# Kernel optimization log

Hardware: AMD Instinct MI355X
Metric: run time of the kernel (lower is better)

The kernel has to match this reference:

```python
import jax, jax.numpy as jnp
import numpy as np

EMBED_DIM = 768
N_HEADS = 12
MLP_HID = 3072  # mlp_ratio 4.0
LN_EPS = 1e-6


def setup_inputs() -> dict:
    key = jax.random.key(0)
    ks = jax.random.split(key, 12)
    B, N, C = 4, 2048, EMBED_DIM
    s = 0.02
    return {
        "x": jax.random.normal(ks[0], (B, N, C), jnp.float32),
        "mask": jnp.ones((B, N), jnp.int32),
        "ln1_g": jnp.ones((C,), jnp.float32),
        "ln1_b": jnp.zeros((C,), jnp.float32),
        "qkv_w": jax.random.normal(ks[1], (C, 3 * C), jnp.float32) * s,
        "qkv_b": jnp.zeros((3 * C,), jnp.float32),
        "proj_w": jax.random.normal(ks[2], (C, C), jnp.float32) * s,
        "proj_b": jnp.zeros((C,), jnp.float32),
        "ln2_g": jnp.ones((C,), jnp.float32),
        "ln2_b": jnp.zeros((C,), jnp.float32),
        "fc1_w": jax.random.normal(ks[3], (C, MLP_HID), jnp.float32) * s,
        "fc1_b": jnp.zeros((MLP_HID,), jnp.float32),
        "fc2_w": jax.random.normal(ks[4], (MLP_HID, C), jnp.float32) * s,
        "fc2_b": jnp.zeros((C,), jnp.float32),
    }


def _layernorm(x, g, b):
    mu = jnp.mean(x, axis=-1, keepdims=True)
    var = jnp.mean(jnp.square(x - mu), axis=-1, keepdims=True)
    return (x - mu) * jax.lax.rsqrt(var + LN_EPS) * g + b


def _block(x, mask, ln1_g, ln1_b, qkv_w, qkv_b, proj_w, proj_b,
           ln2_g, ln2_b, fc1_w, fc1_b, fc2_w, fc2_b):
    B, N, C = x.shape
    H, D = N_HEADS, C // N_HEADS
    scale = D ** -0.5

    # --- attention (pre-norm) ---
    h = _layernorm(x, ln1_g, ln1_b)
    qkv = h @ qkv_w + qkv_b                      # [B,N,3C]
    qkv = qkv.reshape(B, N, 3, H, D).transpose(2, 0, 3, 1, 4)
    q, k, v = qkv[0], qkv[1], qkv[2]             # [B,H,N,D]
    scores = jnp.einsum("bhqd,bhkd->bhqk", q, k * scale)
    # 2-D mask path: (bsz, seq) -> (bsz, 1, seq, 1), mask queries
    m = mask[:, None, :, None]
    scores = jnp.where(m == 0, jnp.finfo(scores.dtype).min, scores)
    attn = jax.nn.softmax(scores, axis=-1)
    vals = jnp.einsum("bhqk,bhkd->bhqd", attn, v)
    vals = vals.transpose(0, 2, 1, 3).reshape(B, N, C)
    x = x + (vals @ proj_w + proj_b)

    # --- MLP (pre-norm, GELU exact) ---
    h = _layernorm(x, ln2_g, ln2_b)
    h = jax.nn.gelu(h @ fc1_w + fc1_b, approximate=False)
    x = x + (h @ fc2_w + fc2_b)
    return x


def reference(x, mask, ln1_g, ln1_b, qkv_w, qkv_b, proj_w, proj_b,
              ln2_g, ln2_b, fc1_w, fc1_b, fc2_w, fc2_b):
    return _block(x, mask, ln1_g, ln1_b, qkv_w, qkv_b, proj_w, proj_b,
                  ln2_g, ln2_b, fc1_w, fc1_b, fc2_w, fc2_b)
```

## Files before the change

### kernel.cpp

```cpp
#include <hip/hip_runtime.h>
#include <hip/hip_bf16.h>
#include <math.h>

using bf16 = __hip_bfloat16;
typedef short s16x8 __attribute__((ext_vector_type(8)));
typedef float f32x4 __attribute__((ext_vector_type(4)));
typedef float f32x16 __attribute__((ext_vector_type(16)));

#define LOG2E 1.4426950408889634f
#define QSCALE 0.18033688f

__device__ inline unsigned short f2bf(float f) {
    bf16 h = __float2bfloat16(f);
    return __builtin_bit_cast(unsigned short, h);
}

__device__ inline void gload_lds16(const void* g, void* l) {
    __builtin_amdgcn_global_load_lds(
        (const __attribute__((address_space(1))) void*)g,
        (__attribute__((address_space(3))) void*)l, 16, 0, 0);
}

__device__ inline unsigned cvtpk(float lo, float hi) {
    unsigned r;
    asm("v_cvt_pk_bf16_f32 %0, %1, %2" : "=v"(r) : "v"(lo), "v"(hi));
    return r;
}

__device__ inline s16x8 build_pfrag(float p0, float p1, float p2, float p3,
                                    float p4, float p5, float p6, float p7) {
    unsigned w01 = cvtpk(p0, p1);
    unsigned w23 = cvtpk(p2, p3);
    unsigned w45 = cvtpk(p4, p5);
    unsigned w67 = cvtpk(p6, p7);
    asm volatile("v_permlane32_swap_b32 %0, %1" : "+v"(w01), "+v"(w45));
    asm volatile("v_permlane32_swap_b32 %0, %1" : "+v"(w23), "+v"(w67));
    int4 t = {(int)w01, (int)w23, (int)w45, (int)w67};
    return __builtin_bit_cast(s16x8, t);
}

__global__ __launch_bounds__(256) void transpose_all(
    const float* __restrict__ qkv_w, const float* __restrict__ proj_w,
    const float* __restrict__ fc1_w, const float* __restrict__ fc2_w,
    bf16* __restrict__ Wqkv, bf16* __restrict__ Wproj,
    bf16* __restrict__ Wfc1, bf16* __restrict__ Wfc2)
{
    int t = blockIdx.x;
    const float* in;
    bf16* out;
    int K, N, xt;
    if (t < 1728)      { in = qkv_w;  out = Wqkv;  K = 768;  N = 2304; xt = 72; }
    else if (t < 2304) { in = proj_w; out = Wproj; K = 768;  N = 768;  xt = 24; t -= 1728; }
    else if (t < 4608) { in = fc1_w;  out = Wfc1;  K = 768;  N = 3072; xt = 96; t -= 2304; }
    else               { in = fc2_w;  out = Wfc2;  K = 3072; N = 768;  xt = 24; t -= 4608; }
    const int bx = (t % xt) * 32;
    const int by = (t / xt) * 32;

    __shared__ float tile[32][33];
    const int tx = threadIdx.x, ty = threadIdx.y;
    #pragma unroll
    for (int i = 0; i < 32; i += 8)
        tile[ty + i][tx] = in[(size_t)(by + ty + i) * N + bx + tx];
    __syncthreads();
    #pragma unroll
    for (int i = 0; i < 32; i += 8)
        out[(size_t)(bx + ty + i) * K + by + tx] = __float2bfloat16(tile[tx][ty + i]);
}

__global__ __launch_bounds__(256) void ln_kernel(
    const float* __restrict__ x, const float* __restrict__ g,
    const float* __restrict__ bb, bf16* __restrict__ out)
{
    const int row = blockIdx.x;
    const float* xr = x + (size_t)row * 768;
    float v[3];
    float s = 0.f, s2 = 0.f;
    #pragma unroll
    for (int i = 0; i < 3; ++i) {
        v[i] = xr[threadIdx.x + i * 256];
        s += v[i];
        s2 += v[i] * v[i];
    }
    #pragma unroll
    for (int off = 1; off < 64; off <<= 1) {
        s += __shfl_xor(s, off);
        s2 += __shfl_xor(s2, off);
    }
    __shared__ float rs[4], rs2[4];
    const int wave = threadIdx.x >> 6;
    if ((threadIdx.x & 63) == 0) { rs[wave] = s; rs2[wave] = s2; }
    __syncthreads();
    s = rs[0] + rs[1] + rs[2] + rs[3];
    s2 = rs2[0] + rs2[1] + rs2[2] + rs2[3];
    const float mu = s * (1.f / 768.f);
    const float var = s2 * (1.f / 768.f) - mu * mu;
    const float r = rsqrtf(var + 1e-6f);
    bf16* orow = out + (size_t)row * 768;
    #pragma unroll
    for (int i = 0; i < 3; ++i) {
        const int col = threadIdx.x + i * 256;
        orow[col] = __float2bfloat16((v[i] - mu) * r * g[col] + bb[col]);
    }
}

template <int EPI>
__global__ __launch_bounds__(256) void gemm_bt(
    const bf16* __restrict__ A, const bf16* __restrict__ Bt,
    const float* __restrict__ bias,
    void* __restrict__ outp, const int* __restrict__ mask,
    bf16* __restrict__ Qb, bf16* __restrict__ Kb, bf16* __restrict__ Vt,
    int M, int N, int K)
{
    __shared__ alignas(16) char smem[32768];
    char* As = smem;
    char* Bs = smem + 16384;
    const int tid = threadIdx.x;
    const int lane = tid & 63;
    const int wave = tid >> 6;
    const int wm = wave >> 1, wn = wave & 1;
    const int lr = lane & 15, lg = lane >> 4;
    const int bm = blockIdx.x, bn = blockIdx.y;

    f32x4 acc[4][4] = {};

    const size_t a_row0 = (size_t)bm * 128;
    const size_t b_row0 = (size_t)bn * 128;

    for (int kt = 0; kt < K; kt += 64) {
        #pragma unroll
        for (int i = 0; i < 4; ++i) {
            const int id = tid + i * 256;
            const int row = id >> 3, c = id & 7;
            const int cs = (c ^ (row & 7)) * 8;
            gload_lds16(A + (a_row0 + row) * K + kt + cs, As + id * 16);
            gload_lds16(Bt + (b_row0 + row) * K + kt + cs, Bs + id * 16);
        }
        __syncthreads();
        #pragma unroll
        for (int ks = 0; ks < 2; ++ks) {
            s16x8 af[4], bfr[4];
            #pragma unroll
            for (int mf = 0; mf < 4; ++mf) {
                const int row = wm * 64 + mf * 16 + lr;
                const int c = ks * 4 + lg;
                af[mf] = *reinterpret_cast<const s16x8*>(As + row * 128 + ((c ^ (row & 7)) * 16));
            }
            #pragma unroll
            for (int nf = 0; nf < 4; ++nf) {
                const int row = wn * 64 + nf * 16 + lr;
                const int c = ks * 4 + lg;
                bfr[nf] = *reinterpret_cast<const s16x8*>(Bs + row * 128 + ((c ^ (row & 7)) * 16));
            }
            #pragma unroll
            for (int mf = 0; mf < 4; ++mf)
                #pragma unroll
                for (int nf = 0; nf < 4; ++nf)
                    acc[mf][nf] = __builtin_amdgcn_mfma_f32_16x16x32_bf16(
                        af[mf], bfr[nf], acc[mf][nf], 0, 0, 0);
        }
        __syncthreads();
    }

    if (EPI == 3) {
        const int rq = bn / 6;
        const int bb_ = bm >> 4;
        if (rq == 2) {
            char* Ws = smem + wave * 8192;
            #pragma unroll
            for (int nf = 0; nf < 4; ++nf) {
                const int cl = nf * 16 + lr;
                const int gn = bn * 128 + wn * 64 + nf * 16 + lr;
                const float bs = bias[gn];
                #pragma unroll
                for (int mf = 0; mf < 4; ++mf) {
                    unsigned short pk[4];
                    #pragma unroll
                    for (int i = 0; i < 4; ++i) pk[i] = f2bf(acc[mf][nf][i] + bs);
                    const int slot = (2 * mf + (lg >> 1)) ^ (cl & 7);
                    *reinterpret_cast<long long*>(Ws + cl * 128 + slot * 16 + (lg & 1) * 8) =
                        *reinterpret_cast<const long long*>(pk);
                }
            }
            __syncthreads();
            const int nb = (bm * 128 + wm * 64) & 2047;
            const int cb = (bn - 12) * 128 + wn * 64;
            #pragma unroll
            for (int r = 0; r < 8; ++r) {
                const int cl = r * 8 + (lane >> 3);
                const int j = lane & 7;
                const int4 vv = *reinterpret_cast<const int4*>(
                    Ws + cl * 128 + ((j ^ (cl & 7)) * 16));
                const int c = cb + cl;
                const int hh = c >> 6, dd = c & 63;
                *reinterpret_cast<int4*>(
                    Vt + ((size_t)(bb_ * 12 + hh) * 64 + dd) * 2048 + nb + j * 8) = vv;
            }
        } else {
            const int cb = bn * 128 - rq * 768 + wn * 64;
            bf16* dst = (rq == 0) ? Qb : Kb;
            #pragma unroll
            for (int mf = 0; mf < 4; ++mf) {
                #pragma unroll
                for (int i = 0; i < 4; ++i) {
                    const int gm = bm * 128 + wm * 64 + mf * 16 + 4 * lg + i;
                    const int n = gm & 2047;
                    const float msc = (rq == 0) ? (mask[gm] ? QSCALE : 0.f) : 1.f;
                    #pragma unroll
                    for (int nf = 0; nf < 4; ++nf) {
                        const int c = cb + nf * 16 + lr;
                        const int h = c >> 6, d = c & 63;
                        const int gn = bn * 128 + wn * 64 + nf * 16 + lr;
                        const float v = (acc[mf][nf][i] + bias[gn]) * msc;
                        dst[((size_t)(bb_ * 12 + h) * 2048 + n) * 64 + d] =
                            __float2bfloat16(v);
                    }
                }
            }
        }
        return;
    }

    #pragma unroll
    for (int mf = 0; mf < 4; ++mf) {
        #pragma unroll
        for (int i = 0; i < 4; ++i) {
            const int gm = bm * 128 + wm * 64 + mf * 16 + 4 * lg + i;
            #pragma unroll
            for (int nf = 0; nf < 4; ++nf) {
                const int gn = bn * 128 + wn * 64 + nf * 16 + lr;
                float v = acc[mf][nf][i] + bias[gn];
                if (EPI == 2) {
                    const float x3 = v * v * v;
                    const float z = fmaf(x3, 0.044715f, v) * 2.3022080f;
                    const float e = __builtin_amdgcn_exp2f(z);
                    v = v - v * __builtin_amdgcn_rcpf(1.f + e);
                }
                reinterpret_cast<bf16*>(outp)[(size_t)gm * N + gn] = __float2bfloat16(v);
            }
        }
    }
}

__global__ __launch_bounds__(256) void gemm64(
    const bf16* __restrict__ A, const bf16* __restrict__ Bt,
    const float* __restrict__ bias, const float* __restrict__ resid,
    float* __restrict__ outp, int M, int N, int K)
{
    __shared__ alignas(16) char smem[24576];
    char* As = smem;
    char* Bs = smem + 8192;
    const int tid = threadIdx.x;
    const int lane = tid & 63;
    const int wn = tid >> 6;
    const int lr = lane & 15, lg = lane >> 4;
    const int bm = blockIdx.x, bn = blockIdx.y;

    f32x4 acc[4][2] = {};

    const size_t a_row0 = (size_t)bm * 64;
    const size_t b_row0 = (size_t)bn * 128;

    for (int kt = 0; kt < K; kt += 64) {
        #pragma unroll
        for (int i = 0; i < 2; ++i) {
            const int id = tid + i * 256;
            const int row = id >> 3, c = id & 7;
            const int cs = (c ^ (row & 7)) * 8;
            gload_lds16(A + (a_row0 + row) * K + kt + cs, As + id * 16);
        }
        #pragma unroll
        for (int i = 0; i < 4; ++i) {
            const int id = tid + i * 256;
            const int row = id >> 3, c = id & 7;
            const int cs = (c ^ (row & 7)) * 8;
            gload_lds16(Bt + (b_row0 + row) * K + kt + cs, Bs + id * 16);
        }
        __syncthreads();
        #pragma unroll
        for (int ks = 0; ks < 2; ++ks) {
            s16x8 af[4], bfr[2];
            #pragma unroll
            for (int mf = 0; mf < 4; ++mf) {
                const int row = mf * 16 + lr;
                const int c = ks * 4 + lg;
                af[mf] = *reinterpret_cast<const s16x8*>(As + row * 128 + ((c ^ (row & 7)) * 16));
            }
            #pragma unroll
            for (int nf = 0; nf < 2; ++nf) {
                const int row = wn * 32 + nf * 16 + lr;
                const int c = ks * 4 + lg;
                bfr[nf] = *reinterpret_cast<const s16x8*>(Bs + row * 128 + ((c ^ (row & 7)) * 16));
            }
            #pragma unroll
            for (int mf = 0; mf < 4; ++mf)
                #pragma unroll
                for (int nf = 0; nf < 2; ++nf)
                    acc[mf][nf] = __builtin_amdgcn_mfma_f32_16x16x32_bf16(
                        af[mf], bfr[nf], acc[mf][nf], 0, 0, 0);
        }
        __syncthreads();
    }

    #pragma unroll
    for (int mf = 0; mf < 4; ++mf) {
        #pragma unroll
        for (int i = 0; i < 4; ++i) {
            const int gm = bm * 64 + mf * 16 + 4 * lg + i;
            #pragma unroll
            for (int nf = 0; nf < 2; ++nf) {
                const int gn = bn * 128 + wn * 32 + nf * 16 + lr;
                outp[(size_t)gm * N + gn] =
                    acc[mf][nf][i] + bias[gn] + resid[(size_t)gm * N + gn];
            }
        }
    }
}

__global__ __launch_bounds__(256, 3) void attn_kernel(
    const bf16* __restrict__ Qb, const bf16* __restrict__ Kb,
    const bf16* __restrict__ Vt, bf16* __restrict__ out)
{
    __shared__ alignas(16) char Ks[2][64 * 128];
    __shared__ alignas(16) char Vs[2][64 * 128];

    const int lin = blockIdx.x;
    const int xcd = lin & 7, slot = lin >> 3;
    const int pair = xcd * 6 + (slot >> 4);
    const int qb = slot & 15;
    const int b = pair / 12, h = pair % 12;

    const int tid = threadIdx.x, lane = tid & 63, wave = tid >> 6;
    const int lq = lane & 31;
    const int hi = lane >> 5;
    const size_t bh = (size_t)(b * 12 + h);
    const bf16* Kh = Kb + bh * 2048 * 64;
    const bf16* Vh = Vt + bh * 64 * 2048;
    const int q0w = qb * 128 + wave * 32;

    s16x8 qf[4];
    {
        const bf16* qp = Qb + (bh * 2048 + q0w + lq) * 64 + 8 * hi;
        #pragma unroll
        for (int ks = 0; ks < 4; ++ks)
            qf[ks] = *reinterpret_cast<const s16x8*>(qp + 16 * ks);
    }
    const int4 onesw = {0x3F803F80, 0x3F803F80, 0x3F803F80, 0x3F803F80};
    const s16x8 onesf = __builtin_bit_cast(s16x8, onesw);

    int sKoff0, sKoff1, dst0, dst1;
    size_t sVoff0, sVoff1;
    {
        const int id0 = tid;
        const int R0 = id0 >> 4;
        const int u0 = (id0 & 15) ^ (R0 & 15);
        const int rt0 = 2 * R0 + (u0 >> 3), s80 = (u0 & 7) * 8;
        sKoff0 = rt0 * 64 + s80;
        sVoff0 = (size_t)rt0 * 2048 + s80;
        dst0 = id0 * 16;
        const int id1 = tid + 256;
        const int R1 = id1 >> 4;
        const int u1 = (id1 & 15) ^ (R1 & 15);
        const int rt1 = 2 * R1 + (u1 >> 3), s81 = (u1 & 7) * 8;
        sKoff1 = rt1 * 64 + s81;
        sVoff1 = (size_t)rt1 * 2048 + s81;
        dst1 = id1 * 16;
    }

    const int rh = lq >> 1;
    const int m7 = rh & 7;
    const int rbase = rh * 256 + (((((lq & 1) << 3) ^ (rh & 8))) << 4);

    f32x16 o0 = {}, o1 = {};
    f32x16 os = {};

    #define STAGE(buf, kb)                                                    \
        do {                                                                  \
            gload_lds16(Kh + (kb) * 4096 + sKoff0, Ks[buf] + dst0);           \
            gload_lds16(Vh + (kb) * 64 + sVoff0, Vs[buf] + dst0);             \
            gload_lds16(Kh + (kb) * 4096 + sKoff1, Ks[buf] + dst1);           \
            gload_lds16(Vh + (kb) * 64 + sVoff1, Vs[buf] + dst1);             \
        } while (0)

    STAGE(0, 0);
    __syncthreads();
    int cur = 0;

    for (int kb = 0; kb < 32; ++kb) {
        if (kb < 31) STAGE(cur ^ 1, kb + 1);
        const char* Kc = Ks[cur] + rbase;
        const char* Vc = Vs[cur] + rbase;

        f32x16 st0 = {}, st1 = {};
        __builtin_amdgcn_s_setprio(1);
        #pragma unroll
        for (int ks = 0; ks < 4; ++ks) {
            const int so = (((2 * ks + hi) ^ m7) << 4);
            const s16x8 kf0 = *reinterpret_cast<const s16x8*>(Kc + so);
            st0 = __builtin_amdgcn_mfma_f32_32x32x16_bf16(kf0, qf[ks], st0, 0, 0, 0);
            const s16x8 kf1 = *reinterpret_cast<const s16x8*>(Kc + 4096 + so);
            st1 = __builtin_amdgcn_mfma_f32_32x32x16_bf16(kf1, qf[ks], st1, 0, 0, 0);
        }
        __builtin_amdgcn_s_setprio(0);

        float p0[16], p1[16];
        #pragma unroll
        for (int r = 0; r < 16; ++r) {
            p0[r] = __builtin_amdgcn_exp2f(st0[r]);
            p1[r] = __builtin_amdgcn_exp2f(st1[r]);
        }

        const s16x8 pf00 = build_pfrag(p0[0], p0[1], p0[2], p0[3], p0[4], p0[5], p0[6], p0[7]);
        const s16x8 pf01 = build_pfrag(p0[8], p0[9], p0[10], p0[11], p0[12], p0[13], p0[14], p0[15]);
        const s16x8 pf10 = build_pfrag(p1[0], p1[1], p1[2], p1[3], p1[4], p1[5], p1[6], p1[7]);
        const s16x8 pf11 = build_pfrag(p1[8], p1[9], p1[10], p1[11], p1[12], p1[13], p1[14], p1[15]);

        __builtin_amdgcn_s_setprio(1);
        #pragma unroll
        for (int kf4 = 0; kf4 < 4; ++kf4) {
            const s16x8 pf = (kf4 == 0) ? pf00 : (kf4 == 1) ? pf01
                           : (kf4 == 2) ? pf10 : pf11;
            const int so = (((2 * kf4 + hi) ^ m7) << 4);
            const s16x8 vf0 = *reinterpret_cast<const s16x8*>(Vc + so);
            o0 = __builtin_amdgcn_mfma_f32_32x32x16_bf16(vf0, pf, o0, 0, 0, 0);
            const s16x8 vf1 = *reinterpret_cast<const s16x8*>(Vc + 4096 + so);
            o1 = __builtin_amdgcn_mfma_f32_32x32x16_bf16(vf1, pf, o1, 0, 0, 0);
            os = __builtin_amdgcn_mfma_f32_32x32x16_bf16(onesf, pf, os, 0, 0, 0);
        }
        __builtin_amdgcn_s_setprio(0);

        __syncthreads();
        cur ^= 1;
    }
    #undef STAGE

    const float rl = 1.0f / os[0];
    bf16* orow = out + (size_t)(b * 2048 + q0w + lq) * 768 + h * 64;
    #pragma unroll
    for (int g = 0; g < 4; ++g) {
        unsigned short pk0[4], pk1[4];
        #pragma unroll
        for (int i = 0; i < 4; ++i) {
            pk0[i] = f2bf(o0[4 * g + i] * rl);
            pk1[i] = f2bf(o1[4 * g + i] * rl);
        }
        const int d0 = 8 * g + 4 * hi;
        *reinterpret_cast<int2*>(orow + d0) = *reinterpret_cast<const int2*>(pk0);
        *reinterpret_cast<int2*>(orow + 32 + d0) = *reinterpret_cast<const int2*>(pk1);
    }
}

extern "C" void kernel_launch(void* const* d_in, const int* in_sizes, int n_in,
                              void* d_out, int out_size, void* d_ws, size_t ws_size,
                              hipStream_t stream)
{
    (void)in_sizes; (void)n_in; (void)out_size; (void)ws_size;
    const float* x      = (const float*)d_in[0];
    const int*   mask   = (const int*)d_in[1];
    const float* ln1_g  = (const float*)d_in[2];
    const float* ln1_b  = (const float*)d_in[3];
    const float* qkv_w  = (const float*)d_in[4];
    const float* qkv_b  = (const float*)d_in[5];
    const float* proj_w = (const float*)d_in[6];
    const float* proj_b = (const float*)d_in[7];
    const float* ln2_g  = (const float*)d_in[8];
    const float* ln2_b  = (const float*)d_in[9];
    const float* fc1_w  = (const float*)d_in[10];
    const float* fc1_b  = (const float*)d_in[11];
    const float* fc2_w  = (const float*)d_in[12];
    const float* fc2_b  = (const float*)d_in[13];
    float* out = (float*)d_out;
    char* ws = (char*)d_ws;

    bf16*  Wt_qkv  = (bf16*)(ws + 0);
    bf16*  Wt_proj = (bf16*)(ws + 3538944);
    bf16*  Wt_fc1  = (bf16*)(ws + 4718592);
    bf16*  Wt_fc2  = (bf16*)(ws + 9437184);
    bf16*  hbuf    = (bf16*)(ws + 14155776);
    bf16*  attnout = (bf16*)(ws + 64487424);
    float* x1      = (float*)(ws + 77070336);
    bf16*  h2      = (bf16*)(ws + 102236160);
    bf16*  a1      = (bf16*)(ws + 114819072);
    bf16*  Qb      = (bf16*)(ws + 114819072);
    bf16*  Kb      = (bf16*)(ws + 127401984);
    bf16*  Vt      = (bf16*)(ws + 139984896);

    transpose_all<<<6912, dim3(32, 8), 0, stream>>>(
        qkv_w, proj_w, fc1_w, fc2_w, Wt_qkv, Wt_proj, Wt_fc1, Wt_fc2);

    ln_kernel<<<8192, 256, 0, stream>>>(x, ln1_g, ln1_b, hbuf);
    gemm_bt<3><<<dim3(64, 18), 256, 0, stream>>>(hbuf, Wt_qkv, qkv_b, nullptr,
                                                 mask, Qb, Kb, Vt, 8192, 2304, 768);
    attn_kernel<<<768, 256, 0, stream>>>(Qb, Kb, Vt, attnout);
    gemm64<<<dim3(128, 6), 256, 0, stream>>>(attnout, Wt_proj, proj_b, x, x1,
                                             8192, 768, 768);
    ln_kernel<<<8192, 256, 0, stream>>>(x1, ln2_g, ln2_b, h2);
    gemm_bt<2><<<dim3(64, 24), 256, 0, stream>>>(h2, Wt_fc1, fc1_b, a1,
                                                 nullptr, nullptr, nullptr, nullptr, 8192, 3072, 768);
    gemm64<<<dim3(128, 6), 256, 0, stream>>>(a1, Wt_fc2, fc2_b, x1, out,
                                             8192, 768, 3072);
}
```

Before: 252.3 us.

## Triple-buffer K/V and compute next block's QK before current PV

The attention loop moves from double to triple LDS buffering, with K/V tiles prefetched two blocks ahead. The QK^T MFMAs for block kb+1 are issued after the exp/pack of block kb and before its PV MFMAs. This software pipelining is meant to let the exp2 and packing VALU work overlap with matrix-core work instead of serialising them. In exchange it raises LDS use to 48KB per block and register pressure from the extra score accumulators, which could hurt occupancy at the three-blocks-per-CU launch bound.

Result: no change. 253.1 us (+0.3%).

```diff
diff --git a/kernel.cpp b/kernel.cpp
--- a/kernel.cpp
+++ b/kernel.cpp
@@ -320,8 +320,8 @@
     const bf16* __restrict__ Qb, const bf16* __restrict__ Kb,
     const bf16* __restrict__ Vt, bf16* __restrict__ out)
 {
-    __shared__ alignas(16) char Ks[2][64 * 128];
-    __shared__ alignas(16) char Vs[2][64 * 128];
+    __shared__ alignas(16) char Ks[3][64 * 128];
+    __shared__ alignas(16) char Vs[3][64 * 128];
 
     const int lin = blockIdx.x;
     const int xcd = lin & 7, slot = lin >> 3;
@@ -381,26 +381,31 @@
             gload_lds16(Vh + (kb) * 64 + sVoff1, Vs[buf] + dst1);             \
         } while (0)
 
+    #define QKCOMP(stv0, stv1, bf)                                            \
+        do {                                                                  \
+            const char* Kc_ = Ks[bf] + rbase;                                 \
+            __builtin_amdgcn_s_setprio(1);                                    \
+            _Pragma("unroll")                                                 \
+            for (int ks = 0; ks < 4; ++ks) {                                  \
+                const int so_ = (((2 * ks + hi) ^ m7) << 4);                  \
+                const s16x8 kf0_ = *reinterpret_cast<const s16x8*>(Kc_ + so_);\
+                stv0 = __builtin_amdgcn_mfma_f32_32x32x16_bf16(kf0_, qf[ks], stv0, 0, 0, 0); \
+                const s16x8 kf1_ = *reinterpret_cast<const s16x8*>(Kc_ + 4096 + so_); \
+                stv1 = __builtin_amdgcn_mfma_f32_32x32x16_bf16(kf1_, qf[ks], stv1, 0, 0, 0); \
+            }                                                                 \
+            __builtin_amdgcn_s_setprio(0);                                    \
+        } while (0)
+
     STAGE(0, 0);
+    STAGE(1, 1);
     __syncthreads();
-    int cur = 0;
+
+    f32x16 st0 = {}, st1 = {};
+    QKCOMP(st0, st1, 0);
 
     for (int kb = 0; kb < 32; ++kb) {
-        if (kb < 31) STAGE(cur ^ 1, kb + 1);
-        const char* Kc = Ks[cur] + rbase;
-        const char* Vc = Vs[cur] + rbase;
-
-        f32x16 st0 = {}, st1 = {};
-        __builtin_amdgcn_s_setprio(1);
-        #pragma unroll
-        for (int ks = 0; ks < 4; ++ks) {
-            const int so = (((2 * ks + hi) ^ m7) << 4);
-            const s16x8 kf0 = *reinterpret_cast<const s16x8*>(Kc + so);
-            st0 = __builtin_amdgcn_mfma_f32_32x32x16_bf16(kf0, qf[ks], st0, 0, 0, 0);
-            const s16x8 kf1 = *reinterpret_cast<const s16x8*>(Kc + 4096 + so);
-            st1 = __builtin_amdgcn_mfma_f32_32x32x16_bf16(kf1, qf[ks], st1, 0, 0, 0);
-        }
-        __builtin_amdgcn_s_setprio(0);
+        const int bV = kb % 3;
+        if (kb < 30) STAGE((kb + 2) % 3, kb + 2);
 
         float p0[16], p1[16];
         #pragma unroll
@@ -408,12 +413,15 @@
             p0[r] = __builtin_amdgcn_exp2f(st0[r]);
             p1[r] = __builtin_amdgcn_exp2f(st1[r]);
         }
-
         const s16x8 pf00 = build_pfrag(p0[0], p0[1], p0[2], p0[3], p0[4], p0[5], p0[6], p0[7]);
         const s16x8 pf01 = build_pfrag(p0[8], p0[9], p0[10], p0[11], p0[12], p0[13], p0[14], p0[15]);
         const s16x8 pf10 = build_pfrag(p1[0], p1[1], p1[2], p1[3], p1[4], p1[5], p1[6], p1[7]);
         const s16x8 pf11 = build_pfrag(p1[8], p1[9], p1[10], p1[11], p1[12], p1[13], p1[14], p1[15]);
 
+        f32x16 nst0 = {}, nst1 = {};
+        if (kb < 31) QKCOMP(nst0, nst1, (kb + 1) % 3);
+
+        const char* Vc = Vs[bV] + rbase;
         __builtin_amdgcn_s_setprio(1);
         #pragma unroll
         for (int kf4 = 0; kf4 < 4; ++kf4) {
@@ -429,9 +437,11 @@
         __builtin_amdgcn_s_setprio(0);
 
         __syncthreads();
-        cur ^= 1;
+        st0 = nst0;
+        st1 = nst1;
     }
     #undef STAGE
+    #undef QKCOMP
 
     const float rl = 1.0f / os[0];
     bf16* orow = out + (size_t)(b * 2048 + q0w + lq) * 768 + h * 64;
```
